# Optimization experiments

Measured on AMD Instinct MI355X. Metric: run time of the kernel, lower is better.

The kernel has to match this reference:

```python
import jax, jax.numpy as jnp
from jax import lax
import numpy as np

B, T, NCLS, D = 64, 2048, 20, 2048
LCS_LEN, FSD_LEN = 64, 32
LAMB1, LAMB2, LAMB3 = 1.0, 5e-5, 8e-5
LAMB_LCS, LAMB_FSD = 0.01, 0.01
FEAT_MARGIN = 50.0
THRES = 0.5
GAMMA = 0.1


def cos_sim(a, b):
    a = a / jnp.linalg.norm(a, axis=1, keepdims=True)
    b = b / jnp.linalg.norm(b, axis=1, keepdims=True)
    return a @ b.T


def dp_fsd(c0, c1):
    # soft-LCS/DTW-style recurrence with maxGamma (soft max) over 3 neighbors
    h = c0.shape[-1] // 2
    m = cos_sim(c0[:, :h], c1[:, :h])  # [L, L]
    g = cos_sim(c0[:, h:], c1[:, h:])  # [L, L]
    L = m.shape[0]

    def row_step(prev_row, mg):
        m_row, g_row = mg
        diag = prev_row[:-1]  # C[i-1, j-1]
        up = prev_row[1:]     # C[i-1, j]

        def col_step(left, xs):  # left = C[i, j-1]
            d, u, mij, gij = xs
            neigh = jnp.stack([d, gij + u, gij + left])
            val = mij + GAMMA * jax.nn.logsumexp(neigh / GAMMA)
            return val, val

        _, row_vals = lax.scan(col_step, jnp.zeros((), m.dtype), (diag, up, m_row, g_row))
        new_row = jnp.concatenate([jnp.zeros((1,), m.dtype), row_vals])
        return new_row, None

    final_row, _ = lax.scan(row_step, jnp.zeros(L + 1, m.dtype), (m, g))
    return final_row[-1]


def dp_lcs(c0, c1):
    s = cos_sim(c0, c1)  # [L, L]
    L = s.shape[0]

    def row_step(prev_row, s_row):
        diag = prev_row[:-1]
        up = prev_row[1:]

        def col_step(left, xs):
            d, u, sij = xs
            val = jnp.where(sij > THRES, d + sij, jnp.maximum(u, left))
            return val, val

        _, row_vals = lax.scan(col_step, jnp.zeros((), s.dtype), (diag, up, s_row))
        return jnp.concatenate([jnp.zeros((1,), s.dtype), row_vals]), None

    final_row, _ = lax.scan(row_step, jnp.zeros(L + 1, s.dtype), s)
    return final_row[-1]


def cls_criterion(p, lab):
    return -jnp.mean(jnp.sum(jnp.log(p + 1e-10) * lab, axis=1))


def forward_once(ai_cls, ac_cls, ab_cls, vlab, att, ai_feat, ac_feat, ab_feat, ai_cas):
    bs = ai_cls.shape[0]
    ones = jnp.ones((bs, 1), ai_cls.dtype)
    zeros = jnp.zeros((bs, 1), ai_cls.dtype)
    inst_lab = jnp.concatenate([vlab, zeros], axis=1)
    cont_lab = jnp.concatenate([vlab, ones], axis=1)
    back_lab = jnp.concatenate([jnp.zeros_like(vlab), ones], axis=1)
    inst_lab = inst_lab / jnp.sum(inst_lab, axis=1, keepdims=True)
    cont_lab = cont_lab / jnp.sum(cont_lab, axis=1, keepdims=True)
    back_lab = back_lab / jnp.sum(back_lab, axis=1, keepdims=True)

    inst_loss = cls_criterion(ai_cls, inst_lab)
    cont_loss = cls_criterion(ac_cls, cont_lab)
    back_loss = cls_criterion(ab_cls, back_lab)

    guide_loss = jnp.mean(jnp.sum(jnp.abs(1.0 - ai_cas[:, :, -1] - lax.stop_gradient(att[:, :, 0])), axis=1))

    n_inst = jnp.linalg.norm(ai_feat, axis=1)
    n_cont = jnp.linalg.norm(ac_feat, axis=1)
    n_back = jnp.linalg.norm(ab_feat, axis=1)
    f1 = jnp.maximum(FEAT_MARGIN - n_inst + n_cont, 0.0)
    f2 = jnp.maximum(FEAT_MARGIN - n_cont + n_back, 0.0)
    f3 = n_back
    feat_loss = jnp.mean((f1 + f2 + f3) ** 2)

    sparse_loss = jnp.mean(jnp.sum(att[:, :, :2], axis=1))

    cls_loss = inst_loss + cont_loss + back_loss  # THUMOS14 weights 1/1/1
    return cls_loss + LAMB1 * guide_loss + LAMB2 * feat_loss + LAMB3 * sparse_loss


def _pair_loss(vals, pair_label):
    bs = vals.shape[0]
    pos = jnp.sum(vals * pair_label)
    neg = jnp.sum(vals * (1.0 - pair_label))
    pos_num = jnp.sum(pair_label)
    neg_num = bs - pos_num
    return neg / (neg_num + 1e-10) - pos / (pos_num + 1e-10)


def ftcl_forward(act_inst_cls_0, act_cont_cls_0, act_back_cls_0, vid_label_0, temp_att_0,
                 act_inst_feat_0, act_cont_feat_0, act_back_feat_0, act_inst_cas_0,
                 lcs_candi_0, fsd_act_candi_0, fsd_bak_candi_0,
                 act_inst_cls_1, act_cont_cls_1, act_back_cls_1, vid_label_1, temp_att_1,
                 act_inst_feat_1, act_cont_feat_1, act_back_feat_1, act_inst_cas_1,
                 lcs_candi_1, fsd_act_candi_1, fsd_bak_candi_1):
    loss_0 = forward_once(act_inst_cls_0, act_cont_cls_0, act_back_cls_0, vid_label_0, temp_att_0,
                          act_inst_feat_0, act_cont_feat_0, act_back_feat_0, act_inst_cas_0)
    loss_1 = forward_once(act_inst_cls_1, act_cont_cls_1, act_back_cls_1, vid_label_1, temp_att_1,
                          act_inst_feat_1, act_cont_feat_1, act_back_feat_1, act_inst_cas_1)
    acm_loss = (loss_0 + loss_1) / 2.0

    pair_label = (jnp.sum(vid_label_0 * vid_label_1, axis=1) > 0).astype(jnp.float32)  # [B]

    lcs = jax.vmap(dp_lcs)(lcs_candi_0, lcs_candi_1)  # [B]
    lcs_loss = _pair_loss(lcs, pair_label)

    # pair==1 -> act_1, pair==0 -> bak_1 (matches the per-sample branch in torch)
    fsd_c1 = jnp.where(pair_label[:, None, None] > 0, fsd_act_candi_1, fsd_bak_candi_1)
    fsd = jax.vmap(dp_fsd)(fsd_act_candi_0, fsd_c1)  # [B]
    fsd_loss = _pair_loss(fsd, pair_label)

    return acm_loss + LAMB_LCS * lcs_loss + LAMB_FSD * fsd_loss


def setup_inputs() -> dict:
    key = jax.random.key(0)
    ks = iter(jax.random.split(key, 32))
    rand = lambda s: jax.random.uniform(next(ks), s, jnp.float32)
    randn = lambda s: jax.random.normal(next(ks), s, jnp.float32)
    inp = {}
    for sfx in ('0', '1'):
        inp[f'act_inst_cls_{sfx}'] = rand((B, NCLS + 1))
        inp[f'act_cont_cls_{sfx}'] = rand((B, NCLS + 1))
        inp[f'act_back_cls_{sfx}'] = rand((B, NCLS + 1))
        inp[f'vid_label_{sfx}'] = jnp.ones((B, NCLS), jnp.float32)
        inp[f'temp_att_{sfx}'] = rand((B, T, 3))
        inp[f'act_inst_feat_{sfx}'] = randn((B, D))
        inp[f'act_cont_feat_{sfx}'] = randn((B, D))
        inp[f'act_back_feat_{sfx}'] = randn((B, D))
        inp[f'act_inst_cas_{sfx}'] = rand((B, T, NCLS + 1))
        inp[f'lcs_candi_{sfx}'] = randn((B, LCS_LEN, D))
        inp[f'fsd_act_candi_{sfx}'] = randn((B, FSD_LEN, D))
        inp[f'fsd_bak_candi_{sfx}'] = randn((B, FSD_LEN, D))
    return inp


def reference(act_inst_cls_0, act_cont_cls_0, act_back_cls_0, vid_label_0, temp_att_0,
              act_inst_feat_0, act_cont_feat_0, act_back_feat_0, act_inst_cas_0,
              lcs_candi_0, fsd_act_candi_0, fsd_bak_candi_0,
              act_inst_cls_1, act_cont_cls_1, act_back_cls_1, vid_label_1, temp_att_1,
              act_inst_feat_1, act_cont_feat_1, act_back_feat_1, act_inst_cas_1,
              lcs_candi_1, fsd_act_candi_1, fsd_bak_candi_1):
    return ftcl_forward(act_inst_cls_0, act_cont_cls_0, act_back_cls_0, vid_label_0, temp_att_0,
                        act_inst_feat_0, act_cont_feat_0, act_back_feat_0, act_inst_cas_0,
                        lcs_candi_0, fsd_act_candi_0, fsd_bak_candi_0,
                        act_inst_cls_1, act_cont_cls_1, act_back_cls_1, vid_label_1, temp_att_1,
                        act_inst_feat_1, act_cont_feat_1, act_back_feat_1, act_inst_cas_1,
                        lcs_candi_1, fsd_act_candi_1, fsd_bak_candi_1)
```

## Files before the change

kernel.cpp:

```cpp
#include <hip/hip_runtime.h>
#include <math.h>

#define Bn 64
#define Tn 2048
#define NCLS 20
#define Dn 2048
#define LCSL 64
#define FSDL 32

typedef __bf16 bf16x4 __attribute__((ext_vector_type(4)));
typedef __bf16 bf16x8 __attribute__((ext_vector_type(8)));
typedef float f32x4 __attribute__((ext_vector_type(4)));

#define WS_LCS 0
#define WS_FSD 64
#define WS_NORM 128
#define WS_GS 512
template <int NS>
struct WsOff {
    static constexpr size_t LSQ = 1024;
    static constexpr size_t FSQ = LSQ + (size_t)64 * NS * 128;
    static constexpr size_t SPART = FSQ + (size_t)64 * NS * 64;
    static constexpr size_t MG = SPART + (size_t)64 * NS * 4096;
    static constexpr size_t END = MG + (size_t)64 * NS * 1024;
};

template <int NS>
__global__ __launch_bounds__(256) void mega_kernel(
    const float* __restrict__ lcs0, const float* __restrict__ lcs1,
    const float* __restrict__ fA0, const float* __restrict__ fA1,
    const float* __restrict__ fB1,
    const float* __restrict__ vid0, const float* __restrict__ vid1,
    const float* __restrict__ cas0, const float* __restrict__ att0,
    const float* __restrict__ cas1, const float* __restrict__ att1,
    const float* __restrict__ f0, const float* __restrict__ f1,
    const float* __restrict__ f2, const float* __restrict__ f3,
    const float* __restrict__ f4, const float* __restrict__ f5,
    float* __restrict__ ws) {
    constexpr int L = (NS == 16) ? 4 : 3;
    constexpr int KC = 2048 / NS / 64;
    using O = WsOff<NS>;
    __shared__ __align__(16) __bf16 tA[2][4096];
    __shared__ __align__(16) __bf16 tB[2][4096];
    const int t = threadIdx.x;
    const int bid = blockIdx.x;
    const int w = t >> 6, lane = t & 63;
    const int quad = lane >> 4, l16 = lane & 15;

    if (bid < 64 * NS) {
        const int b = bid >> L, ks = bid & (NS - 1);
        const float* c0 = lcs0 + (size_t)b * LCSL * Dn + ks * (2048 / NS);
        const float* c1 = lcs1 + (size_t)b * LCSL * Dn + ks * (2048 / NS);

        f32x4 acc[4] = {};
        float sqa[4] = {0.f, 0.f, 0.f, 0.f}, sqb[4] = {0.f, 0.f, 0.f, 0.f};
        float4 pA[4], pB[4];

        auto LOADL = [&](int st) {
            #pragma unroll
            for (int l = 0; l < 4; ++l) {
                int idx4 = l * 256 + t;
                int row = idx4 >> 4, kq4 = idx4 & 15;
                pA[l] = *(const float4*)(c0 + (size_t)row * Dn + st * 64 + kq4 * 4);
                pB[l] = *(const float4*)(c1 + (size_t)row * Dn + st * 64 + kq4 * 4);
            }
        };
        auto WRITEL = [&](int buf) {
            #pragma unroll
            for (int l = 0; l < 4; ++l) {
                int idx4 = l * 256 + t;
                int row = idx4 >> 4, kq4 = idx4 & 15;
                int c = kq4 >> 1, h = kq4 & 1;
                int pos = row * 64 + ((c ^ (row & 7)) << 3) + h * 4;
                float4 av = pA[l], bv = pB[l];
                bf16x4 a4 = {(__bf16)av.x, (__bf16)av.y, (__bf16)av.z, (__bf16)av.w};
                bf16x4 b4 = {(__bf16)bv.x, (__bf16)bv.y, (__bf16)bv.z, (__bf16)bv.w};
                *(bf16x4*)&tA[buf][pos] = a4;
                *(bf16x4*)&tB[buf][pos] = b4;
                sqa[l] += av.x * av.x + av.y * av.y + av.z * av.z + av.w * av.w;
                sqb[l] += bv.x * bv.x + bv.y * bv.y + bv.z * bv.z + bv.w * bv.w;
            }
        };

        LOADL(0);
        WRITEL(0);
        if (KC > 1) LOADL(1);
        __syncthreads();
        for (int kc = 0; kc < KC; ++kc) {
            const int cur = kc & 1;
            #pragma unroll
            for (int s = 0; s < 2; ++s) {
                int ar = w * 16 + l16;
                int ac_ = (s * 4 + quad) ^ (ar & 7);
                bf16x8 af = *(const bf16x8*)&tA[cur][ar * 64 + (ac_ << 3)];
                #pragma unroll
                for (int tj = 0; tj < 4; ++tj) {
                    int br = tj * 16 + l16;
                    int bc = (s * 4 + quad) ^ (br & 7);
                    bf16x8 bf = *(const bf16x8*)&tB[cur][br * 64 + (bc << 3)];
                    acc[tj] = __builtin_amdgcn_mfma_f32_16x16x32_bf16(af, bf, acc[tj], 0, 0, 0);
                }
            }
            if (kc + 1 < KC) {
                WRITEL(cur ^ 1);
                if (kc + 2 < KC) LOADL(kc + 2);
                __syncthreads();
            }
        }
        float* dst = ws + O::SPART + (size_t)(b * NS + ks) * 4096;
        #pragma unroll
        for (int tj = 0; tj < 4; ++tj)
            #pragma unroll
            for (int rg = 0; rg < 4; ++rg)
                dst[(w * 16 + quad * 4 + rg) * 64 + tj * 16 + l16] = acc[tj][rg];
        #pragma unroll
        for (int l = 0; l < 4; ++l) {
            float sa = sqa[l], sb = sqb[l];
            #pragma unroll
            for (int m = 1; m < 16; m <<= 1) {
                sa += __shfl_xor(sa, m);
                sb += __shfl_xor(sb, m);
            }
            if ((t & 15) == 0) {
                int r = l * 16 + (t >> 4);
                float* q = ws + O::LSQ + (size_t)(b * NS + ks) * 128;
                q[r] = sa;
                q[64 + r] = sb;
            }
        }
    } else if (bid < 128 * NS) {
        const int qb = bid - 64 * NS;
        const int b = qb >> L;
        const int idx = qb & (NS - 1);
        const int half = idx >> (L - 1);
        const int ks = idx & (NS / 2 - 1);
        float ps = 0.f;
        for (int c = 0; c < NCLS; ++c) ps += vid0[b * NCLS + c] * vid1[b * NCLS + c];
        const float* base1 = (ps > 0.f) ? fA1 : fB1;
        const float* c0 = fA0 + (size_t)b * FSDL * Dn + half * 1024 + ks * (2048 / NS);
        const float* c1 = base1 + (size_t)b * FSDL * Dn + half * 1024 + ks * (2048 / NS);
        const int wi = w >> 1, wj = w & 1;

        f32x4 acc = {};
        float sqa[2] = {0.f, 0.f}, sqb[2] = {0.f, 0.f};
        float4 pA[2], pB[2];

        auto LOADF = [&](int st) {
            #pragma unroll
            for (int l = 0; l < 2; ++l) {
                int idx4 = l * 256 + t;
                int row = idx4 >> 4, kq4 = idx4 & 15;
                pA[l] = *(const float4*)(c0 + (size_t)row * Dn + st * 64 + kq4 * 4);
                pB[l] = *(const float4*)(c1 + (size_t)row * Dn + st * 64 + kq4 * 4);
            }
        };
        auto WRITEF = [&](int buf) {
            #pragma unroll
            for (int l = 0; l < 2; ++l) {
                int idx4 = l * 256 + t;
                int row = idx4 >> 4, kq4 = idx4 & 15;
                int c = kq4 >> 1, h = kq4 & 1;
                int pos = row * 64 + ((c ^ (row & 7)) << 3) + h * 4;
                float4 av = pA[l], bv = pB[l];
                bf16x4 a4 = {(__bf16)av.x, (__bf16)av.y, (__bf16)av.z, (__bf16)av.w};
                bf16x4 b4 = {(__bf16)bv.x, (__bf16)bv.y, (__bf16)bv.z, (__bf16)bv.w};
                *(bf16x4*)&tA[buf][pos] = a4;
                *(bf16x4*)&tB[buf][pos] = b4;
                sqa[l] += av.x * av.x + av.y * av.y + av.z * av.z + av.w * av.w;
                sqb[l] += bv.x * bv.x + bv.y * bv.y + bv.z * bv.z + bv.w * bv.w;
            }
        };

        LOADF(0);
        WRITEF(0);
        if (KC > 1) LOADF(1);
        __syncthreads();
        for (int kc = 0; kc < KC; ++kc) {
            const int cur = kc & 1;
            #pragma unroll
            for (int s = 0; s < 2; ++s) {
                int ar = wi * 16 + l16;
                int ac_ = (s * 4 + quad) ^ (ar & 7);
                bf16x8 af = *(const bf16x8*)&tA[cur][ar * 64 + (ac_ << 3)];
                int br = wj * 16 + l16;
                int bc = (s * 4 + quad) ^ (br & 7);
                bf16x8 bf = *(const bf16x8*)&tB[cur][br * 64 + (bc << 3)];
                acc = __builtin_amdgcn_mfma_f32_16x16x32_bf16(af, bf, acc, 0, 0, 0);
            }
            if (kc + 1 < KC) {
                WRITEF(cur ^ 1);
                if (kc + 2 < KC) LOADF(kc + 2);
                __syncthreads();
            }
        }
        float* dst = ws + O::MG + (size_t)((b * 2 + half) * (NS / 2) + ks) * 1024;
        #pragma unroll
        for (int rg = 0; rg < 4; ++rg)
            dst[(wi * 16 + quad * 4 + rg) * 32 + wj * 16 + l16] = acc[rg];
        #pragma unroll
        for (int l = 0; l < 2; ++l) {
            float sa = sqa[l], sb = sqb[l];
            #pragma unroll
            for (int m = 1; m < 16; m <<= 1) {
                sa += __shfl_xor(sa, m);
                sb += __shfl_xor(sb, m);
            }
            if ((t & 15) == 0) {
                int r = l * 16 + (t >> 4);
                float* qq = ws + O::FSQ + (size_t)((b * 2 + half) * (NS / 2) + ks) * 64;
                qq[r] = sa;
                qq[32 + r] = sb;
            }
        }
    } else if (bid < 128 * NS + 128) {
        const int gb = bid - 128 * NS;
        const int N = Bn * Tn;
        float g0 = 0.f, s0 = 0.f, g1 = 0.f, s1 = 0.f;
        for (int n = gb * 256 + t; n < 2 * N; n += 128 * 256) {
            int sfx = (n >= N);
            int m = sfx ? (n - N) : n;
            const float* cas = sfx ? cas1 : cas0;
            const float* att = sfx ? att1 : att0;
            float a0 = att[m * 3 + 0];
            float a1 = att[m * 3 + 1];
            float g = fabsf(1.0f - cas[m * (NCLS + 1) + NCLS] - a0);
            float s = a0 + a1;
            if (sfx) { g1 += g; s1 += s; } else { g0 += g; s0 += s; }
        }
        float* red = (float*)tA;
        float vals[4] = {g0, s0, g1, s1};
        #pragma unroll
        for (int v = 0; v < 4; ++v) red[v * 256 + t] = vals[v];
        __syncthreads();
        for (int o = 128; o; o >>= 1) {
            if (t < o) {
                #pragma unroll
                for (int v = 0; v < 4; ++v) red[v * 256 + t] += red[v * 256 + t + o];
            }
            __syncthreads();
        }
        if (t < 4) ws[WS_GS + gb * 4 + t] = red[t * 256];
    } else {
        int R = (bid - (128 * NS + 128)) * 4 + w;
        const float* arr[6] = {f0, f1, f2, f3, f4, f5};
        const float* p = arr[R >> 6] + (size_t)(R & 63) * Dn;
        float s = 0.f;
        #pragma unroll
        for (int qd = 0; qd < 8; ++qd) {
            float4 v = *(const float4*)(p + qd * 256 + lane * 4);
            s += v.x * v.x + v.y * v.y + v.z * v.z + v.w * v.w;
        }
        for (int off = 32; off; off >>= 1) s += __shfl_down(s, off);
        if (lane == 0) ws[WS_NORM + R] = sqrtf(s);
    }
}

template <int NS>
__global__ __launch_bounds__(256) void dp_kernel(float* __restrict__ ws) {
    using O = WsOff<NS>;
    const int t = threadIdx.x;
    if (blockIdx.x < 64) {
        const int b = blockIdx.x;
        __shared__ float S[64 * 68];
        __shared__ float inv[128];
        if (t < 128) {
            float s = 0.f;
            #pragma unroll
            for (int ks = 0; ks < NS; ++ks)
                s += ws[O::LSQ + (size_t)(b * NS + ks) * 128 + t];
            inv[t] = 1.0f / sqrtf(s);
        }
        __syncthreads();
        const float* sp = ws + O::SPART + (size_t)b * NS * 4096;
        #pragma unroll
        for (int qd = 0; qd < 4; ++qd) {
            int idx4 = qd * 256 + t;
            int i = idx4 >> 4, j = (idx4 & 15) * 4;
            float4 v = {0.f, 0.f, 0.f, 0.f};
            #pragma unroll
            for (int ks = 0; ks < NS; ++ks) {
                float4 p = *(const float4*)(sp + (size_t)ks * 4096 + idx4 * 4);
                v.x += p.x; v.y += p.y; v.z += p.z; v.w += p.w;
            }
            float ri = inv[i];
            S[i * 68 + j + 0] = v.x * ri * inv[64 + j + 0];
            S[i * 68 + j + 1] = v.y * ri * inv[64 + j + 1];
            S[i * 68 + j + 2] = v.z * ri * inv[64 + j + 2];
            S[i * 68 + j + 3] = v.w * ri * inv[64 + j + 3];
        }
        __syncthreads();
        if (t < 64) {
            float prev = 0.f, prevprev = 0.f;
            float sval_next = S[t * 68 + 0];
            for (int d = 2; d <= 128; ++d) {
                float s = sval_next;
                int jn = d - t - 1;
                if (jn >= 0 && jn < 64) sval_next = S[t * 68 + jn];
                float up = __shfl_up(prev, 1);
                float dg = __shfl_up(prevprev, 1);
                if (t == 0) { up = 0.f; dg = 0.f; }
                int j = d - t - 1;
                float left = prev;
                float val = (s > 0.5f) ? (dg + s) : fmaxf(up, left);
                float cur = (j >= 1 && j <= 64) ? val : 0.f;
                prevprev = prev;
                prev = cur;
            }
            if (t == 63) ws[WS_LCS + b] = prev;
        }
    } else {
        const int b = blockIdx.x - 64;
        __shared__ float M[32 * 36], G[32 * 36];
        __shared__ float inv[128];
        if (t < 128) {
            int half = t >> 6, sub = t & 63;
            float s = 0.f;
            #pragma unroll
            for (int ks = 0; ks < NS / 2; ++ks)
                s += ws[O::FSQ + (size_t)((b * 2 + half) * (NS / 2) + ks) * 64 + sub];
            inv[t] = 1.0f / sqrtf(s);
        }
        __syncthreads();
        {
            int idx4 = t;
            int i = idx4 >> 3, j = (idx4 & 7) * 4;
            float4 vM = {0.f, 0.f, 0.f, 0.f}, vG = {0.f, 0.f, 0.f, 0.f};
            #pragma unroll
            for (int ks = 0; ks < NS / 2; ++ks) {
                float4 pM = *(const float4*)(ws + O::MG + (size_t)((b * 2 + 0) * (NS / 2) + ks) * 1024 + idx4 * 4);
                float4 pG = *(const float4*)(ws + O::MG + (size_t)((b * 2 + 1) * (NS / 2) + ks) * 1024 + idx4 * 4);
                vM.x += pM.x; vM.y += pM.y; vM.z += pM.z; vM.w += pM.w;
                vG.x += pG.x; vG.y += pG.y; vG.z += pG.z; vG.w += pG.w;
            }
            float riM = inv[i], riG = inv[64 + i];
            M[i * 36 + j + 0] = vM.x * riM * inv[32 + j + 0];
            M[i * 36 + j + 1] = vM.y * riM * inv[32 + j + 1];
            M[i * 36 + j + 2] = vM.z * riM * inv[32 + j + 2];
            M[i * 36 + j + 3] = vM.w * riM * inv[32 + j + 3];
            G[i * 36 + j + 0] = vG.x * riG * inv[96 + j + 0];
            G[i * 36 + j + 1] = vG.y * riG * inv[96 + j + 1];
            G[i * 36 + j + 2] = vG.z * riG * inv[96 + j + 2];
            G[i * 36 + j + 3] = vG.w * riG * inv[96 + j + 3];
        }
        __syncthreads();
        if (t < 32) {
            float prev = 0.f, prevprev = 0.f;
            float m_next = M[t * 36 + 0], g_next = G[t * 36 + 0];
            for (int d = 2; d <= 64; ++d) {
                float m = m_next, g = g_next;
                int jn = d - t - 1;
                if (jn >= 0 && jn < 32) { m_next = M[t * 36 + jn]; g_next = G[t * 36 + jn]; }
                float up = __shfl_up(prev, 1);
                float dg = __shfl_up(prevprev, 1);
                if (t == 0) { up = 0.f; dg = 0.f; }
                int j = d - t - 1;
                float left = prev;
                float x0 = dg * 10.0f;
                float x1 = (g + up) * 10.0f;
                float x2 = (g + left) * 10.0f;
                float mx = fmaxf(x0, fmaxf(x1, x2));
                float lse = mx + __logf(__expf(x0 - mx) + __expf(x1 - mx) + __expf(x2 - mx));
                float val = m + 0.1f * lse;
                float cur = (j >= 1 && j <= 32) ? val : 0.f;
                prevprev = prev;
                prev = cur;
            }
            if (t == 31) ws[WS_FSD + b] = prev;
        }
    }
}

__device__ __forceinline__ float4 block_reduce4(float4 v, float4* red, int t) {
    red[t] = v;
    __syncthreads();
    for (int o = 128; o; o >>= 1) {
        if (t < o) {
            red[t].x += red[t + o].x;
            red[t].y += red[t + o].y;
            red[t].z += red[t + o].z;
            red[t].w += red[t + o].w;
        }
        __syncthreads();
    }
    float4 r = red[0];
    __syncthreads();
    return r;
}

__global__ __launch_bounds__(256) void final_kernel(
    const float* __restrict__ ai0, const float* __restrict__ ac0,
    const float* __restrict__ ab0, const float* __restrict__ vid0,
    const float* __restrict__ ai1, const float* __restrict__ ac1,
    const float* __restrict__ ab1, const float* __restrict__ vid1,
    const float* __restrict__ ws, float* __restrict__ out) {
    __shared__ float rs0[Bn], rs1[Bn], plsh[Bn];
    __shared__ __align__(16) float4 red[256];
    int t = threadIdx.x;
    if (t < Bn) {
        float s0 = 0.f, s1 = 0.f, pp = 0.f;
        for (int c = 0; c < NCLS; ++c) {
            float a = vid0[t * NCLS + c], bl = vid1[t * NCLS + c];
            s0 += a; s1 += bl; pp += a * bl;
        }
        rs0[t] = s0;
        rs1[t] = s1;
        plsh[t] = (pp > 0.f) ? 1.f : 0.f;
    }
    __syncthreads();

    float inst0 = 0.f, cont0 = 0.f, back0 = 0.f;
    float inst1 = 0.f, cont1 = 0.f, back1 = 0.f;
    for (int idx = t; idx < Bn * (NCLS + 1); idx += 256) {
        int b = idx / (NCLS + 1), c = idx % (NCLS + 1);
        float v0 = (c < NCLS) ? vid0[b * NCLS + c] : 0.f;
        float v1 = (c < NCLS) ? vid1[b * NCLS + c] : 0.f;
        float wI0 = (c < NCLS) ? (v0 / rs0[b]) : 0.f;
        float wC0 = ((c < NCLS) ? v0 : 1.f) / (rs0[b] + 1.f);
        float wI1 = (c < NCLS) ? (v1 / rs1[b]) : 0.f;
        float wC1 = ((c < NCLS) ? v1 : 1.f) / (rs1[b] + 1.f);
        inst0 += logf(ai0[idx] + 1e-10f) * wI0;
        cont0 += logf(ac0[idx] + 1e-10f) * wC0;
        inst1 += logf(ai1[idx] + 1e-10f) * wI1;
        cont1 += logf(ac1[idx] + 1e-10f) * wC1;
        if (c == NCLS) {
            back0 += logf(ab0[idx] + 1e-10f);
            back1 += logf(ab1[idx] + 1e-10f);
        }
    }

    float g0 = 0.f, s0v = 0.f, g1 = 0.f, s1v = 0.f;
    for (int i = t; i < 128; i += 256) {
        g0  += ws[WS_GS + i * 4 + 0];
        s0v += ws[WS_GS + i * 4 + 1];
        g1  += ws[WS_GS + i * 4 + 2];
        s1v += ws[WS_GS + i * 4 + 3];
    }

    float fv0 = 0.f, fv1 = 0.f;
    if (t < Bn) {
        const float* nm = ws + WS_NORM;
        {
            float ni = nm[0 * Bn + t], nc = nm[1 * Bn + t], nb = nm[2 * Bn + t];
            float f1 = fmaxf(50.0f - ni + nc, 0.f);
            float f2 = fmaxf(50.0f - nc + nb, 0.f);
            float f = f1 + f2 + nb;
            fv0 = f * f;
        }
        {
            float ni = nm[3 * Bn + t], nc = nm[4 * Bn + t], nb = nm[5 * Bn + t];
            float f1 = fmaxf(50.0f - ni + nc, 0.f);
            float f2 = fmaxf(50.0f - nc + nb, 0.f);
            float f = f1 + f2 + nb;
            fv1 = f * f;
        }
    }

    float posL = 0.f, negL = 0.f, posF = 0.f, negF = 0.f, pln = 0.f;
    if (t < Bn) {
        float pl = plsh[t];
        float lv = ws[WS_LCS + t];
        float fv = ws[WS_FSD + t];
        posL = lv * pl; negL = lv * (1.f - pl);
        posF = fv * pl; negF = fv * (1.f - pl);
        pln = pl;
    }

    float4 r1 = block_reduce4({inst0, cont0, back0, inst1}, red, t);
    float4 r2 = block_reduce4({cont1, back1, g0, s0v}, red, t);
    float4 r3 = block_reduce4({g1, s1v, fv0, fv1}, red, t);
    float4 r4 = block_reduce4({posL, negL, posF, negF}, red, t);
    float4 r5 = block_reduce4({pln, 0.f, 0.f, 0.f}, red, t);

    if (t == 0) {
        float cls0 = -(r1.x + r1.y + r1.z) / (float)Bn;
        float cls1 = -(r1.w + r2.x + r2.y) / (float)Bn;
        float guide0 = r2.z / (float)Bn;
        float sparse0 = r2.w / (float)(Bn * 2);
        float guide1 = r3.x / (float)Bn;
        float sparse1 = r3.y / (float)(Bn * 2);
        float sFeat0 = r3.z / (float)Bn;
        float sFeat1 = r3.w / (float)Bn;
        float loss0 = cls0 + 1.0f * guide0 + 5e-05f * sFeat0 + 8e-05f * sparse0;
        float loss1 = cls1 + 1.0f * guide1 + 5e-05f * sFeat1 + 8e-05f * sparse1;
        float acm = 0.5f * (loss0 + loss1);
        float posn = r5.x;
        float negn = (float)Bn - posn;
        float lcs_loss = r4.y / (negn + 1e-10f) - r4.x / (posn + 1e-10f);
        float fsd_loss = r4.w / (negn + 1e-10f) - r4.z / (posn + 1e-10f);
        out[0] = acm + 0.01f * lcs_loss + 0.01f * fsd_loss;
    }
}

extern "C" void kernel_launch(void* const* d_in, const int* in_sizes, int n_in,
                              void* d_out, int out_size, void* d_ws, size_t ws_size,
                              hipStream_t stream) {
    (void)in_sizes; (void)n_in; (void)out_size;
    const float* ai0  = (const float*)d_in[0];
    const float* ac0  = (const float*)d_in[1];
    const float* ab0  = (const float*)d_in[2];
    const float* vid0 = (const float*)d_in[3];
    const float* att0 = (const float*)d_in[4];
    const float* fi0  = (const float*)d_in[5];
    const float* fc0  = (const float*)d_in[6];
    const float* fb0  = (const float*)d_in[7];
    const float* cas0 = (const float*)d_in[8];
    const float* lcs0 = (const float*)d_in[9];
    const float* fsdA0 = (const float*)d_in[10];
    const float* ai1  = (const float*)d_in[12];
    const float* ac1  = (const float*)d_in[13];
    const float* ab1  = (const float*)d_in[14];
    const float* vid1 = (const float*)d_in[15];
    const float* att1 = (const float*)d_in[16];
    const float* fi1  = (const float*)d_in[17];
    const float* fc1  = (const float*)d_in[18];
    const float* fb1  = (const float*)d_in[19];
    const float* cas1 = (const float*)d_in[20];
    const float* lcs1 = (const float*)d_in[21];
    const float* fsdA1 = (const float*)d_in[22];
    const float* fsdB1 = (const float*)d_in[23];

    float* ws = (float*)d_ws;

    if (ws_size >= WsOff<16>::END * sizeof(float)) {
        mega_kernel<16><<<128 * 16 + 224, 256, 0, stream>>>(
            lcs0, lcs1, fsdA0, fsdA1, fsdB1, vid0, vid1, cas0, att0, cas1, att1,
            fi0, fc0, fb0, fi1, fc1, fb1, ws);
        dp_kernel<16><<<128, 256, 0, stream>>>(ws);
    } else {
        mega_kernel<8><<<128 * 8 + 224, 256, 0, stream>>>(
            lcs0, lcs1, fsdA0, fsdA1, fsdB1, vid0, vid1, cas0, att0, cas1, att1,
            fi0, fc0, fb0, fi1, fc1, fb1, ws);
        dp_kernel<8><<<128, 256, 0, stream>>>(ws);
    }
    final_kernel<<<1, 256, 0, stream>>>(ai0, ac0, ab0, vid0, ai1, ac1, ab1, vid1, ws,
                                        (float*)d_out);
}
```

Measured before the change: 236.0 us.

## Reorder mega-kernel blocks and move final-loss reductions into dp_kernel

The long-running global-sum and feature-norm blocks are moved to the front of the mega-kernel grid so they start first instead of trailing the matmul blocks. The classification-loss, guide/sparse and feature-margin reductions move out of the single-block final kernel into three extra dp_kernel blocks, where they run alongside the DP recurrences. The final kernel becomes a 64-thread wave-shuffle reduction that reads precomputed scalars, and shared-memory tree reductions are replaced by wave shuffles. This shortens the serial tail after the DP kernel, at the cost of more workspace slots and a more complex block-dispatch layout.

```diff
diff --git a/kernel.cpp b/kernel.cpp
--- a/kernel.cpp
+++ b/kernel.cpp
@@ -22,8 +22,12 @@
     static constexpr size_t FSQ = LSQ + (size_t)64 * NS * 128;
     static constexpr size_t SPART = FSQ + (size_t)64 * NS * 64;
     static constexpr size_t MG = SPART + (size_t)64 * NS * 4096;
-    static constexpr size_t END = MG + (size_t)64 * NS * 1024;
+    static constexpr size_t SC = MG + (size_t)64 * NS * 1024;
+    static constexpr size_t PL = SC + 16;
+    static constexpr size_t END = PL + 64;
 };
+
+#define AUXB 224
 
 template <int NS>
 __global__ __launch_bounds__(256) void mega_kernel(
@@ -47,8 +51,49 @@
     const int w = t >> 6, lane = t & 63;
     const int quad = lane >> 4, l16 = lane & 15;
 
-    if (bid < 64 * NS) {
-        const int b = bid >> L, ks = bid & (NS - 1);
+    if (bid < 128) {
+        const int gb = bid;
+        const int N = Bn * Tn;
+        float g0 = 0.f, s0 = 0.f, g1 = 0.f, s1 = 0.f;
+        for (int n = gb * 256 + t; n < 2 * N; n += 128 * 256) {
+            int sfx = (n >= N);
+            int m = sfx ? (n - N) : n;
+            const float* cas = sfx ? cas1 : cas0;
+            const float* att = sfx ? att1 : att0;
+            float a0 = att[m * 3 + 0];
+            float a1 = att[m * 3 + 1];
+            float g = fabsf(1.0f - cas[m * (NCLS + 1) + NCLS] - a0);
+            float s = a0 + a1;
+            if (sfx) { g1 += g; s1 += s; } else { g0 += g; s0 += s; }
+        }
+        float* red = (float*)tA;
+        float vals[4] = {g0, s0, g1, s1};
+        #pragma unroll
+        for (int v = 0; v < 4; ++v) red[v * 256 + t] = vals[v];
+        __syncthreads();
+        for (int o = 128; o; o >>= 1) {
+            if (t < o) {
+                #pragma unroll
+                for (int v = 0; v < 4; ++v) red[v * 256 + t] += red[v * 256 + t + o];
+            }
+            __syncthreads();
+        }
+        if (t < 4) ws[WS_GS + gb * 4 + t] = red[t * 256];
+    } else if (bid < AUXB) {
+        int R = (bid - 128) * 4 + w;
+        const float* arr[6] = {f0, f1, f2, f3, f4, f5};
+        const float* p = arr[R >> 6] + (size_t)(R & 63) * Dn;
+        float s = 0.f;
+        #pragma unroll
+        for (int qd = 0; qd < 8; ++qd) {
+            float4 v = *(const float4*)(p + qd * 256 + lane * 4);
+            s += v.x * v.x + v.y * v.y + v.z * v.z + v.w * v.w;
+        }
+        for (int off = 32; off; off >>= 1) s += __shfl_down(s, off);
+        if (lane == 0) ws[WS_NORM + R] = sqrtf(s);
+    } else if (bid < AUXB + 64 * NS) {
+        const int gb = bid - AUXB;
+        const int b = gb >> L, ks = gb & (NS - 1);
         const float* c0 = lcs0 + (size_t)b * LCSL * Dn + ks * (2048 / NS);
         const float* c1 = lcs1 + (size_t)b * LCSL * Dn + ks * (2048 / NS);
 
@@ -128,8 +173,8 @@
                 q[64 + r] = sb;
             }
         }
-    } else if (bid < 128 * NS) {
-        const int qb = bid - 64 * NS;
+    } else {
+        const int qb = bid - AUXB - 64 * NS;
         const int b = qb >> L;
         const int idx = qb & (NS - 1);
         const int half = idx >> (L - 1);
@@ -212,51 +257,35 @@
                 qq[32 + r] = sb;
             }
         }
-    } else if (bid < 128 * NS + 128) {
-        const int gb = bid - 128 * NS;
-        const int N = Bn * Tn;
-        float g0 = 0.f, s0 = 0.f, g1 = 0.f, s1 = 0.f;
-        for (int n = gb * 256 + t; n < 2 * N; n += 128 * 256) {
-            int sfx = (n >= N);
-            int m = sfx ? (n - N) : n;
-            const float* cas = sfx ? cas1 : cas0;
-            const float* att = sfx ? att1 : att0;
-            float a0 = att[m * 3 + 0];
-            float a1 = att[m * 3 + 1];
-            float g = fabsf(1.0f - cas[m * (NCLS + 1) + NCLS] - a0);
-            float s = a0 + a1;
-            if (sfx) { g1 += g; s1 += s; } else { g0 += g; s0 += s; }
-        }
-        float* red = (float*)tA;
-        float vals[4] = {g0, s0, g1, s1};
-        #pragma unroll
-        for (int v = 0; v < 4; ++v) red[v * 256 + t] = vals[v];
-        __syncthreads();
-        for (int o = 128; o; o >>= 1) {
-            if (t < o) {
-                #pragma unroll
-                for (int v = 0; v < 4; ++v) red[v * 256 + t] += red[v * 256 + t + o];
-            }
-            __syncthreads();
-        }
-        if (t < 4) ws[WS_GS + gb * 4 + t] = red[t * 256];
-    } else {
-        int R = (bid - (128 * NS + 128)) * 4 + w;
-        const float* arr[6] = {f0, f1, f2, f3, f4, f5};
-        const float* p = arr[R >> 6] + (size_t)(R & 63) * Dn;
-        float s = 0.f;
-        #pragma unroll
-        for (int qd = 0; qd < 8; ++qd) {
-            float4 v = *(const float4*)(p + qd * 256 + lane * 4);
-            s += v.x * v.x + v.y * v.y + v.z * v.z + v.w * v.w;
-        }
-        for (int off = 32; off; off >>= 1) s += __shfl_down(s, off);
-        if (lane == 0) ws[WS_NORM + R] = sqrtf(s);
     }
 }
 
+__device__ __forceinline__ float4 wbr4(float4 v, float4* redw, int t) {
+    #pragma unroll
+    for (int m = 1; m < 64; m <<= 1) {
+        v.x += __shfl_xor(v.x, m);
+        v.y += __shfl_xor(v.y, m);
+        v.z += __shfl_xor(v.z, m);
+        v.w += __shfl_xor(v.w, m);
+    }
+    if ((t & 63) == 0) redw[t >> 6] = v;
+    __syncthreads();
+    float4 r;
+    r.x = redw[0].x + redw[1].x + redw[2].x + redw[3].x;
+    r.y = redw[0].y + redw[1].y + redw[2].y + redw[3].y;
+    r.z = redw[0].z + redw[1].z + redw[2].z + redw[3].z;
+    r.w = redw[0].w + redw[1].w + redw[2].w + redw[3].w;
+    __syncthreads();
+    return r;
+}
+
 template <int NS>
-__global__ __launch_bounds__(256) void dp_kernel(float* __restrict__ ws) {
+__global__ __launch_bounds__(256) void dp_kernel(
+    float* __restrict__ ws,
+    const float* __restrict__ ai0, const float* __restrict__ ac0,
+    const float* __restrict__ ab0, const float* __restrict__ vid0,
+    const float* __restrict__ ai1, const float* __restrict__ ac1,
+    const float* __restrict__ ab1, const float* __restrict__ vid1) {
     using O = WsOff<NS>;
     const int t = threadIdx.x;
     if (blockIdx.x < 64) {
@@ -308,7 +337,7 @@
             }
             if (t == 63) ws[WS_LCS + b] = prev;
         }
-    } else {
+    } else if (blockIdx.x < 128) {
         const int b = blockIdx.x - 64;
         __shared__ float M[32 * 36], G[32 * 36];
         __shared__ float inv[128];
@@ -367,126 +396,117 @@
             }
             if (t == 31) ws[WS_FSD + b] = prev;
         }
+    } else if (blockIdx.x == 128) {
+        __shared__ float rs0[Bn], rs1[Bn];
+        __shared__ __align__(16) float4 redw[4];
+        float plreg = 0.f;
+        if (t < Bn) {
+            float s0 = 0.f, s1 = 0.f, pp = 0.f;
+            for (int c = 0; c < NCLS; ++c) {
+                float a = vid0[t * NCLS + c], bl = vid1[t * NCLS + c];
+                s0 += a; s1 += bl; pp += a * bl;
+            }
+            rs0[t] = s0;
+            rs1[t] = s1;
+            plreg = (pp > 0.f) ? 1.f : 0.f;
+            ws[O::PL + t] = plreg;
+        }
+        __syncthreads();
+        float inst0 = 0.f, cont0 = 0.f, back0 = 0.f;
+        float inst1 = 0.f, cont1 = 0.f, back1 = 0.f;
+        for (int idx = t; idx < Bn * (NCLS + 1); idx += 256) {
+            int b = idx / (NCLS + 1), c = idx % (NCLS + 1);
+            float v0 = (c < NCLS) ? vid0[b * NCLS + c] : 0.f;
+            float v1 = (c < NCLS) ? vid1[b * NCLS + c] : 0.f;
+            float wI0 = (c < NCLS) ? (v0 / rs0[b]) : 0.f;
+            float wC0 = ((c < NCLS) ? v0 : 1.f) / (rs0[b] + 1.f);
+            float wI1 = (c < NCLS) ? (v1 / rs1[b]) : 0.f;
+            float wC1 = ((c < NCLS) ? v1 : 1.f) / (rs1[b] + 1.f);
+            inst0 += logf(ai0[idx] + 1e-10f) * wI0;
+            cont0 += logf(ac0[idx] + 1e-10f) * wC0;
+            inst1 += logf(ai1[idx] + 1e-10f) * wI1;
+            cont1 += logf(ac1[idx] + 1e-10f) * wC1;
+            if (c == NCLS) {
+                back0 += logf(ab0[idx] + 1e-10f);
+                back1 += logf(ab1[idx] + 1e-10f);
+            }
+        }
+        float4 r1 = wbr4({inst0, cont0, back0, inst1}, redw, t);
+        float4 r2 = wbr4({cont1, back1, plreg, 0.f}, redw, t);
+        if (t == 0) {
+            ws[O::SC + 0] = r1.x; ws[O::SC + 1] = r1.y; ws[O::SC + 2] = r1.z;
+            ws[O::SC + 3] = r1.w; ws[O::SC + 4] = r2.x; ws[O::SC + 5] = r2.y;
+            ws[O::SC + 12] = r2.z;
+        }
+    } else if (blockIdx.x == 129) {
+        __shared__ __align__(16) float4 redw[4];
+        float4 g = {0.f, 0.f, 0.f, 0.f};
+        if (t < 128) g = *(const float4*)&ws[WS_GS + t * 4];
+        float4 r = wbr4(g, redw, t);
+        if (t == 0) {
+            ws[O::SC + 6] = r.x; ws[O::SC + 7] = r.y;
+            ws[O::SC + 8] = r.z; ws[O::SC + 9] = r.w;
+        }
+    } else if (blockIdx.x == 130) {
+        __shared__ __align__(16) float4 redw[4];
+        float fv0 = 0.f, fv1 = 0.f;
+        if (t < Bn) {
+            const float* nm = ws + WS_NORM;
+            {
+                float ni = nm[0 * Bn + t], nc = nm[1 * Bn + t], nb = nm[2 * Bn + t];
+                float f1 = fmaxf(50.0f - ni + nc, 0.f);
+                float f2 = fmaxf(50.0f - nc + nb, 0.f);
+                float f = f1 + f2 + nb;
+                fv0 = f * f;
+            }
+            {
+                float ni = nm[3 * Bn + t], nc = nm[4 * Bn + t], nb = nm[5 * Bn + t];
+                float f1 = fmaxf(50.0f - ni + nc, 0.f);
+                float f2 = fmaxf(50.0f - nc + nb, 0.f);
+                float f = f1 + f2 + nb;
+                fv1 = f * f;
+            }
+        }
+        float4 r = wbr4({fv0, fv1, 0.f, 0.f}, redw, t);
+        if (t == 0) {
+            ws[O::SC + 10] = r.x; ws[O::SC + 11] = r.y;
+        }
     }
 }
 
-__device__ __forceinline__ float4 block_reduce4(float4 v, float4* red, int t) {
-    red[t] = v;
-    __syncthreads();
-    for (int o = 128; o; o >>= 1) {
-        if (t < o) {
-            red[t].x += red[t + o].x;
-            red[t].y += red[t + o].y;
-            red[t].z += red[t + o].z;
-            red[t].w += red[t + o].w;
-        }
-        __syncthreads();
+template <int NS>
+__global__ __launch_bounds__(64) void final_kernel(const float* __restrict__ ws,
+                                                   float* __restrict__ out) {
+    using O = WsOff<NS>;
+    const int t = threadIdx.x;
+    float pl = ws[O::PL + t];
+    float lv = ws[WS_LCS + t];
+    float fv = ws[WS_FSD + t];
+    float4 v = {lv * pl, lv * (1.f - pl), fv * pl, fv * (1.f - pl)};
+    #pragma unroll
+    for (int m = 1; m < 64; m <<= 1) {
+        v.x += __shfl_xor(v.x, m);
+        v.y += __shfl_xor(v.y, m);
+        v.z += __shfl_xor(v.z, m);
+        v.w += __shfl_xor(v.w, m);
     }
-    float4 r = red[0];
-    __syncthreads();
-    return r;
-}
-
-__global__ __launch_bounds__(256) void final_kernel(
-    const float* __restrict__ ai0, const float* __restrict__ ac0,
-    const float* __restrict__ ab0, const float* __restrict__ vid0,
-    const float* __restrict__ ai1, const float* __restrict__ ac1,
-    const float* __restrict__ ab1, const float* __restrict__ vid1,
-    const float* __restrict__ ws, float* __restrict__ out) {
-    __shared__ float rs0[Bn], rs1[Bn], plsh[Bn];
-    __shared__ __align__(16) float4 red[256];
-    int t = threadIdx.x;
-    if (t < Bn) {
-        float s0 = 0.f, s1 = 0.f, pp = 0.f;
-        for (int c = 0; c < NCLS; ++c) {
-            float a = vid0[t * NCLS + c], bl = vid1[t * NCLS + c];
-            s0 += a; s1 += bl; pp += a * bl;
-        }
-        rs0[t] = s0;
-        rs1[t] = s1;
-        plsh[t] = (pp > 0.f) ? 1.f : 0.f;
-    }
-    __syncthreads();
-
-    float inst0 = 0.f, cont0 = 0.f, back0 = 0.f;
-    float inst1 = 0.f, cont1 = 0.f, back1 = 0.f;
-    for (int idx = t; idx < Bn * (NCLS + 1); idx += 256) {
-        int b = idx / (NCLS + 1), c = idx % (NCLS + 1);
-        float v0 = (c < NCLS) ? vid0[b * NCLS + c] : 0.f;
-        float v1 = (c < NCLS) ? vid1[b * NCLS + c] : 0.f;
-        float wI0 = (c < NCLS) ? (v0 / rs0[b]) : 0.f;
-        float wC0 = ((c < NCLS) ? v0 : 1.f) / (rs0[b] + 1.f);
-        float wI1 = (c < NCLS) ? (v1 / rs1[b]) : 0.f;
-        float wC1 = ((c < NCLS) ? v1 : 1.f) / (rs1[b] + 1.f);
-        inst0 += logf(ai0[idx] + 1e-10f) * wI0;
-        cont0 += logf(ac0[idx] + 1e-10f) * wC0;
-        inst1 += logf(ai1[idx] + 1e-10f) * wI1;
-        cont1 += logf(ac1[idx] + 1e-10f) * wC1;
-        if (c == NCLS) {
-            back0 += logf(ab0[idx] + 1e-10f);
-            back1 += logf(ab1[idx] + 1e-10f);
-        }
-    }
-
-    float g0 = 0.f, s0v = 0.f, g1 = 0.f, s1v = 0.f;
-    for (int i = t; i < 128; i += 256) {
-        g0  += ws[WS_GS + i * 4 + 0];
-        s0v += ws[WS_GS + i * 4 + 1];
-        g1  += ws[WS_GS + i * 4 + 2];
-        s1v += ws[WS_GS + i * 4 + 3];
-    }
-
-    float fv0 = 0.f, fv1 = 0.f;
-    if (t < Bn) {
-        const float* nm = ws + WS_NORM;
-        {
-            float ni = nm[0 * Bn + t], nc = nm[1 * Bn + t], nb = nm[2 * Bn + t];
-            float f1 = fmaxf(50.0f - ni + nc, 0.f);
-            float f2 = fmaxf(50.0f - nc + nb, 0.f);
-            float f = f1 + f2 + nb;
-            fv0 = f * f;
-        }
-        {
-            float ni = nm[3 * Bn + t], nc = nm[4 * Bn + t], nb = nm[5 * Bn + t];
-            float f1 = fmaxf(50.0f - ni + nc, 0.f);
-            float f2 = fmaxf(50.0f - nc + nb, 0.f);
-            float f = f1 + f2 + nb;
-            fv1 = f * f;
-        }
-    }
-
-    float posL = 0.f, negL = 0.f, posF = 0.f, negF = 0.f, pln = 0.f;
-    if (t < Bn) {
-        float pl = plsh[t];
-        float lv = ws[WS_LCS + t];
-        float fv = ws[WS_FSD + t];
-        posL = lv * pl; negL = lv * (1.f - pl);
-        posF = fv * pl; negF = fv * (1.f - pl);
-        pln = pl;
-    }
-
-    float4 r1 = block_reduce4({inst0, cont0, back0, inst1}, red, t);
-    float4 r2 = block_reduce4({cont1, back1, g0, s0v}, red, t);
-    float4 r3 = block_reduce4({g1, s1v, fv0, fv1}, red, t);
-    float4 r4 = block_reduce4({posL, negL, posF, negF}, red, t);
-    float4 r5 = block_reduce4({pln, 0.f, 0.f, 0.f}, red, t);
-
     if (t == 0) {
-        float cls0 = -(r1.x + r1.y + r1.z) / (float)Bn;
-        float cls1 = -(r1.w + r2.x + r2.y) / (float)Bn;
-        float guide0 = r2.z / (float)Bn;
-        float sparse0 = r2.w / (float)(Bn * 2);
-        float guide1 = r3.x / (float)Bn;
-        float sparse1 = r3.y / (float)(Bn * 2);
-        float sFeat0 = r3.z / (float)Bn;
-        float sFeat1 = r3.w / (float)Bn;
+        const float* sc = ws + O::SC;
+        float cls0 = -(sc[0] + sc[1] + sc[2]) / (float)Bn;
+        float cls1 = -(sc[3] + sc[4] + sc[5]) / (float)Bn;
+        float guide0 = sc[6] / (float)Bn;
+        float sparse0 = sc[7] / (float)(Bn * 2);
+        float guide1 = sc[8] / (float)Bn;
+        float sparse1 = sc[9] / (float)(Bn * 2);
+        float sFeat0 = sc[10] / (float)Bn;
+        float sFeat1 = sc[11] / (float)Bn;
         float loss0 = cls0 + 1.0f * guide0 + 5e-05f * sFeat0 + 8e-05f * sparse0;
         float loss1 = cls1 + 1.0f * guide1 + 5e-05f * sFeat1 + 8e-05f * sparse1;
         float acm = 0.5f * (loss0 + loss1);
-        float posn = r5.x;
+        float posn = sc[12];
         float negn = (float)Bn - posn;
-        float lcs_loss = r4.y / (negn + 1e-10f) - r4.x / (posn + 1e-10f);
-        float fsd_loss = r4.w / (negn + 1e-10f) - r4.z / (posn + 1e-10f);
+        float lcs_loss = v.y / (negn + 1e-10f) - v.x / (posn + 1e-10f);
+        float fsd_loss = v.w / (negn + 1e-10f) - v.z / (posn + 1e-10f);
         out[0] = acm + 0.01f * lcs_loss + 0.01f * fsd_loss;
     }
 }
@@ -522,16 +542,16 @@
     float* ws = (float*)d_ws;
 
     if (ws_size >= WsOff<16>::END * sizeof(float)) {
-        mega_kernel<16><<<128 * 16 + 224, 256, 0, stream>>>(
+        mega_kernel<16><<<AUXB + 128 * 16, 256, 0, stream>>>(
             lcs0, lcs1, fsdA0, fsdA1, fsdB1, vid0, vid1, cas0, att0, cas1, att1,
             fi0, fc0, fb0, fi1, fc1, fb1, ws);
-        dp_kernel<16><<<128, 256, 0, stream>>>(ws);
+        dp_kernel<16><<<131, 256, 0, stream>>>(ws, ai0, ac0, ab0, vid0, ai1, ac1, ab1, vid1);
+        final_kernel<16><<<1, 64, 0, stream>>>(ws, (float*)d_out);
     } else {
-        mega_kernel<8><<<128 * 8 + 224, 256, 0, stream>>>(
+        mega_kernel<8><<<AUXB + 128 * 8, 256, 0, stream>>>(
             lcs0, lcs1, fsdA0, fsdA1, fsdB1, vid0, vid1, cas0, att0, cas1, att1,
             fi0, fc0, fb0, fi1, fc1, fb1, ws);
-        dp_kernel<8><<<128, 256, 0, stream>>>(ws);
+        dp_kernel<8><<<131, 256, 0, stream>>>(ws, ai0, ac0, ab0, vid0, ai1, ac1, ab1, vid1);
+        final_kernel<8><<<1, 64, 0, stream>>>(ws, (float*)d_out);
     }
-    final_kernel<<<1, 256, 0, stream>>>(ai0, ac0, ab0, vid0, ai1, ac1, ab1, vid1, ws,
-                                        (float*)d_out);
 }
```

Result: faster. 224.5 us (-4.9%).
